# Kernel tuning notes

Measured on AMD Instinct MI355X. Metric: run time of the kernel, lower is better.

Reference implementation:

```python
import jax, jax.numpy as jnp
import numpy as np

B, S, E, H, MLP = 2, 2048, 1024, 16, 4096
VEC = 8          # args.vec_length: block-row height of vector-sparse mask
SPARSITY = 0.9   # fraction of attention entries dropped
D = E // H


def _make_mask():
    # static_random_mask_aligned: each block-row of VEC query rows keeps a
    # random ~(1-sparsity) subset of key columns. Diagonal kept so every
    # softmax row is non-empty.
    rng = np.random.default_rng(0)
    block = rng.random((S // VEC, S)) < (1.0 - SPARSITY)   # [m, n]
    mask = np.repeat(block, VEC, axis=0)                   # [S, S]
    mask |= np.eye(S, dtype=bool)
    return jnp.asarray(mask)


def setup_inputs() -> dict:
    key = jax.random.key(0)
    ks = jax.random.split(key, 8)
    w = lambda k, shp: (0.02 * jax.random.normal(k, shp, dtype=jnp.float32))
    return {
        "x": jax.random.normal(ks[0], (B, S, E), dtype=jnp.float32),
        "mask": _make_mask(),                       # [S,S] bool, static
        "w_qkv": w(ks[1], (3 * E, E)),             # in_proj_weight
        "b_qkv": jnp.zeros((3 * E,), jnp.float32),
        "w_out": w(ks[2], (E, E)),                 # out_proj
        "b_out": jnp.zeros((E,), jnp.float32),
        "g1": jnp.ones((E,), jnp.float32), "beta1": jnp.zeros((E,), jnp.float32),
        "g2": jnp.ones((E,), jnp.float32), "beta2": jnp.zeros((E,), jnp.float32),
        "w1": w(ks[3], (MLP, E)), "bias1": jnp.zeros((MLP,), jnp.float32),
        "w2": w(ks[4], (E, MLP)), "bias2": jnp.zeros((E,), jnp.float32),
    }


def _layer_norm(x, g, b, eps=1e-5):
    mu = jnp.mean(x, axis=-1, keepdims=True)
    var = jnp.mean(jnp.square(x - mu), axis=-1, keepdims=True)
    return (x - mu) * jax.lax.rsqrt(var + eps) * g + b


def _sparse_mha(h, mask, w_qkv, b_qkv, w_out, b_out):
    qkv = jnp.einsum("bse,fe->bsf", h, w_qkv) + b_qkv       # [B,S,3E]
    q, k, v = jnp.split(qkv, 3, axis=-1)
    q = q.reshape(B, S, H, D)
    k = k.reshape(B, S, H, D)
    v = v.reshape(B, S, H, D)
    scores = jnp.einsum("bqhd,bkhd->bhqk", q, k) / jnp.sqrt(jnp.float32(D))
    scores = jnp.where(mask[None, None], scores, jnp.float32(-1e9))
    p = jax.nn.softmax(scores, axis=-1)
    ctx = jnp.einsum("bhqk,bkhd->bqhd", p, v).reshape(B, S, E)
    return jnp.einsum("bse,fe->bsf", ctx, w_out) + b_out


def reference(x, mask, w_qkv, b_qkv, w_out, b_out, g1, beta1, g2, beta2,
              w1, bias1, w2, bias2):
    h = _layer_norm(x, g1, beta1)
    attn = _sparse_mha(h, mask, w_qkv, b_qkv, w_out, b_out)
    out = attn + x                      # residual 1
    out = _layer_norm(out, g2, beta2)
    out = jnp.einsum("bse,me->bsm", out, w1) + bias1   # linear1 (no activation, as in source)
    out = jnp.einsum("bsm,em->bse", out, w2) + bias2   # linear2
    return out + x                      # residual adds ORIGINAL x (as in source)
```

## Files before the change

### kernel.cpp

```cpp
#include <hip/hip_runtime.h>
#include <cstdint>
#include <cstddef>

typedef unsigned short u16;
typedef unsigned int u32;
typedef short s16x8 __attribute__((ext_vector_type(8)));
typedef float f32x4 __attribute__((ext_vector_type(4)));
typedef _Float16 f16x2 __attribute__((ext_vector_type(2)));

__device__ __forceinline__ float fdot2(f16x2 a, f16x2 b, float c) {
#if defined(__HIP_DEVICE_COMPILE__) && __has_builtin(__builtin_amdgcn_fdot2)
  return __builtin_amdgcn_fdot2(a, b, c, false);
#else
  return (float)a.x * (float)b.x + (float)a.y * (float)b.y + c;
#endif
}

__device__ __forceinline__ float red8(float x) {
#if defined(__HIP_DEVICE_COMPILE__)
  asm("v_add_f32_dpp %0, %0, %0 quad_perm:[1,0,3,2] row_mask:0xf bank_mask:0xf"
      : "+v"(x));
  asm("v_add_f32_dpp %0, %0, %0 quad_perm:[2,3,0,1] row_mask:0xf bank_mask:0xf"
      : "+v"(x));
  asm("v_add_f32_dpp %0, %0, %0 row_half_mirror row_mask:0xf bank_mask:0xf"
      : "+v"(x));
  return x;
#else
  x += __shfl_xor(x, 1); x += __shfl_xor(x, 2); x += __shfl_xor(x, 4);
  return x;
#endif
}

__device__ __forceinline__ void fmamix_lo(float& a, u32 hv, float p) {
#if defined(__HIP_DEVICE_COMPILE__)
  asm("v_fma_mix_f32 %0, %1, %2, %0 op_sel_hi:[1,0,0]"
      : "+v"(a) : "v"(hv), "v"(p));
#else
  union { u32 i; _Float16 h[2]; } c; c.i = hv; a += (float)c.h[0] * p;
#endif
}
__device__ __forceinline__ void fmamix_hi(float& a, u32 hv, float p) {
#if defined(__HIP_DEVICE_COMPILE__)
  asm("v_fma_mix_f32 %0, %1, %2, %0 op_sel:[1,0,0] op_sel_hi:[1,0,0]"
      : "+v"(a) : "v"(hv), "v"(p));
#else
  union { u32 i; _Float16 h[2]; } c; c.i = hv; a += (float)c.h[1] * p;
#endif
}

#define S_LEN 2048
#define EMB   1024
#define NHEAD 16
#define HD    64
#define E3    3072
#define MLPD  4096
#define NROWS 4096
#define LCAP  640

__device__ __forceinline__ float bf2f(u16 v) {
  union { u32 i; float f; } c; c.i = ((u32)v) << 16; return c.f;
}
__device__ __forceinline__ u16 f2bf(float f) {
  union { float f; u32 i; } c; c.f = f;
  u32 x = c.i;
  return (u16)((x + 0x7FFFu + ((x >> 16) & 1u)) >> 16);
}
__device__ __forceinline__ u16 f2h(float f) {
  _Float16 h = (_Float16)f;
  union { _Float16 h; u16 b; } c; c.h = h; return c.b;
}

__device__ __forceinline__ void gl2lds16(const void* g, void* l) {
  __builtin_amdgcn_global_load_lds(
      (__attribute__((address_space(1))) void*)(g),
      (__attribute__((address_space(3))) void*)(l), 16, 0, 0);
}

__global__ void detect_flags(const u32* __restrict__ w1s, int* __restrict__ dtflag,
                             const u32* __restrict__ mask, int* __restrict__ maskrep) {
  __shared__ int hits[256];
  __shared__ u32 red[256];
  int h = 0; u32 v = 0;
  for (int i = threadIdx.x; i < 4096; i += 256) {
    u32 w = w1s[i];
    if ((w & 0xFFFFu) && (((w >> 7) & 0xFFu) >= 0xC8u)) ++h;
    v |= mask[i];
  }
  hits[threadIdx.x] = h; red[threadIdx.x] = v;
  __syncthreads();
  if (threadIdx.x == 0) {
    int t = 0; u32 o = 0;
    for (int i = 0; i < 256; ++i) { t += hits[i]; o |= red[i]; }
    *dtflag = (t > 8) ? 1 : 0;
    int rep;
    if (o <= 1u) rep = 0;
    else if (o & 0x80u) rep = 1;
    else if (o & 0x00800000u) rep = 2;
    else rep = 3;
    *maskrep = rep;
  }
}

__device__ __forceinline__ bool maskbit(const void* m, int rep, size_t idx) {
  switch (rep) {
    case 0:  return ((const int*)m)[idx] != 0;
    case 1:  return ((const u16*)m)[idx] != 0;
    case 2:  return ((const u32*)m)[idx] != 0;
    default: return ((const unsigned char*)m)[idx] != 0;
  }
}

__global__ __launch_bounds__(256)
void cvt_kernel(const void* __restrict__ src, u16* __restrict__ dst,
                int n8, const int* __restrict__ dtflag) {
  const int i = blockIdx.x * blockDim.x + threadIdx.x;
  if (i >= n8) return;
  if (*dtflag) {
    const float4 a = ((const float4*)src)[i * 2];
    const float4 b = ((const float4*)src)[i * 2 + 1];
    u16 o[8] = {f2bf(a.x), f2bf(a.y), f2bf(a.z), f2bf(a.w),
                f2bf(b.x), f2bf(b.y), f2bf(b.z), f2bf(b.w)};
    *(uint4*)(dst + (size_t)i * 8) = *(const uint4*)o;
  } else {
    ((uint4*)dst)[i] = ((const uint4*)src)[i];
  }
}

__global__ void cvt_small(const void* s0, u16* d0, const void* s1, u16* d1,
                          const void* s2, u16* d2, const void* s3, u16* d3,
                          const void* s4, u16* d4, const void* s5, u16* d5,
                          const void* s6, u16* d6, const void* s7, u16* d7,
                          const int* __restrict__ dtflag) {
  const int f = *dtflag;
  const void* srcs[8] = {s0, s1, s2, s3, s4, s5, s6, s7};
  u16* dsts[8] = {d0, d1, d2, d3, d4, d5, d6, d7};
  const int ns[8] = {E3, EMB, EMB, EMB, EMB, EMB, MLPD, EMB};
#pragma unroll
  for (int k = 0; k < 8; ++k) {
    for (int idx = threadIdx.x; idx < ns[k]; idx += 256)
      dsts[k][idx] = f ? f2bf(((const float*)srcs[k])[idx])
                       : ((const u16*)srcs[k])[idx];
  }
}

__global__ void build_lists(const void* __restrict__ mask, const int* __restrict__ repf,
                            int* __restrict__ lists, int* __restrict__ cnt,
                            unsigned char* __restrict__ diagflag) {
  __shared__ int num;
  const int m = blockIdx.x;
  if (threadIdx.x == 0) num = 0;
  __syncthreads();
  const int rep = *repf;
  const int row0 = m * 8;
  for (int j = threadIdx.x; j < S_LEN; j += 256) {
    int srcrow = (j == row0) ? (row0 + 1) : row0;
    bool bit = maskbit(mask, rep, (size_t)srcrow * S_LEN + j);
    if (j >= row0 && j < row0 + 8) diagflag[j] = bit ? 0 : 1;
    if (bit) {
      int p = atomicAdd(&num, 1);
      if (p < LCAP) lists[m * LCAP + p] = j * 4096;
    }
  }
  __syncthreads();
  if (threadIdx.x == 0) cnt[m] = (num < LCAP) ? num : LCAP;
}

__global__ __launch_bounds__(256)
void ln_kernel(const void* __restrict__ Xv, const u16* __restrict__ g,
               const u16* __restrict__ be, u16* __restrict__ O,
               const int* __restrict__ inf32) {
  const int wv = threadIdx.x >> 6, ln = threadIdx.x & 63;
  const int row = blockIdx.x * 4 + wv;
  float v[16];
  if (inf32 && *inf32) {
    const float* xr = (const float*)Xv + (size_t)row * EMB;
    float4 a0 = *(const float4*)(xr + ln * 8);
    float4 a1 = *(const float4*)(xr + ln * 8 + 4);
    float4 b0 = *(const float4*)(xr + 512 + ln * 8);
    float4 b1 = *(const float4*)(xr + 512 + ln * 8 + 4);
    v[0]=a0.x; v[1]=a0.y; v[2]=a0.z; v[3]=a0.w; v[4]=a1.x; v[5]=a1.y; v[6]=a1.z; v[7]=a1.w;
    v[8]=b0.x; v[9]=b0.y; v[10]=b0.z; v[11]=b0.w; v[12]=b1.x; v[13]=b1.y; v[14]=b1.z; v[15]=b1.w;
  } else {
    const u16* xr = (const u16*)Xv + (size_t)row * EMB;
    union { uint4 u; u16 s[8]; } p0, p1;
    p0.u = *(const uint4*)(xr + ln * 8);
    p1.u = *(const uint4*)(xr + 512 + ln * 8);
#pragma unroll
    for (int t = 0; t < 8; ++t) { v[t] = bf2f(p0.s[t]); v[8 + t] = bf2f(p1.s[t]); }
  }
  float s = 0.f, sq = 0.f;
#pragma unroll
  for (int t = 0; t < 16; ++t) { s += v[t]; sq += v[t] * v[t]; }
#pragma unroll
  for (int off = 32; off; off >>= 1) { s += __shfl_xor(s, off); sq += __shfl_xor(sq, off); }
  const float mu = s * (1.0f / EMB);
  const float var = sq * (1.0f / EMB) - mu * mu;
  const float rsig = rsqrtf(var + 1e-5f);
  union { uint4 u; u16 s[8]; } g0, g1v, b0, b1v, o0, o1;
  g0.u = *(const uint4*)(g + ln * 8);   g1v.u = *(const uint4*)(g + 512 + ln * 8);
  b0.u = *(const uint4*)(be + ln * 8);  b1v.u = *(const uint4*)(be + 512 + ln * 8);
#pragma unroll
  for (int t = 0; t < 8; ++t) {
    o0.s[t] = f2bf((v[t]     - mu) * rsig * bf2f(g0.s[t])  + bf2f(b0.s[t]));
    o1.s[t] = f2bf((v[8 + t] - mu) * rsig * bf2f(g1v.s[t]) + bf2f(b1v.s[t]));
  }
  u16* orow = O + (size_t)row * EMB;
  *(uint4*)(orow + ln * 8) = o0.u;
  *(uint4*)(orow + 512 + ln * 8) = o1.u;
}

__global__ __launch_bounds__(256)
void gemm_bt(const u16* __restrict__ A, const u16* __restrict__ B,
             const u16* __restrict__ bias, u16* __restrict__ C,
             int M, int N, int K) {
  __shared__ u16 a_sh[128 * 64];
  __shared__ u16 b_sh[128 * 64];
  const int tid = threadIdx.x;
  const int wv = tid >> 6, ln = tid & 63;
  const int wm = wv & 1, wn = wv >> 1;
  const int tm = blockIdx.y, tn = blockIdx.x;
  const int srow = ln >> 3;
  const int scol = ((ln & 7) ^ srow) * 8;
  const int q = ln >> 4, rr = ln & 15;

  f32x4 acc[4][4] = {};
  const u16* Abase = A + (size_t)(tm * 128) * K;
  const u16* Bbase = B + (size_t)(tn * 128) * K;

  for (int k0 = 0; k0 < K; k0 += 64) {
    __syncthreads();
#pragma unroll
    for (int c = 0; c < 4; ++c) {
      const int chunk = wv * 4 + c;
      const int row = chunk * 8 + srow;
      gl2lds16(Abase + (size_t)row * K + k0 + scol, &a_sh[chunk * 512]);
      gl2lds16(Bbase + (size_t)row * K + k0 + scol, &b_sh[chunk * 512]);
    }
    __syncthreads();
#pragma unroll
    for (int kk = 0; kk < 2; ++kk) {
      const int slot = ((kk * 4 + q) ^ (rr & 7)) * 8;
      s16x8 af[4], bfr[4];
#pragma unroll
      for (int mi = 0; mi < 4; ++mi)
        af[mi] = *(const s16x8*)&a_sh[(wm * 64 + mi * 16 + rr) * 64 + slot];
#pragma unroll
      for (int ni = 0; ni < 4; ++ni)
        bfr[ni] = *(const s16x8*)&b_sh[(wn * 64 + ni * 16 + rr) * 64 + slot];
#pragma unroll
      for (int mi = 0; mi < 4; ++mi)
#pragma unroll
        for (int ni = 0; ni < 4; ++ni)
          acc[mi][ni] = __builtin_amdgcn_mfma_f32_16x16x32_bf16(af[mi], bfr[ni], acc[mi][ni], 0, 0, 0);
    }
  }
#pragma unroll
  for (int ni = 0; ni < 4; ++ni) {
    const int col = tn * 128 + wn * 64 + ni * 16 + rr;
    const float bv = bf2f(bias[col]);
#pragma unroll
    for (int mi = 0; mi < 4; ++mi)
#pragma unroll
      for (int r2 = 0; r2 < 4; ++r2) {
        const int row = tm * 128 + wm * 64 + mi * 16 + q * 4 + r2;
        C[(size_t)row * N + col] = f2bf(acc[mi][ni][r2] + bv);
      }
  }
}

__global__ __launch_bounds__(256)
void gemm_bt_sk(const u16* __restrict__ A, const u16* __restrict__ B,
                u16* __restrict__ P0, u16* __restrict__ P1,
                int M, int N, int K) {
  __shared__ u16 a_sh[128 * 64];
  __shared__ u16 b_sh[128 * 64];
  const int tid = threadIdx.x;
  const int wv = tid >> 6, ln = tid & 63;
  const int wm = wv & 1, wn = wv >> 1;
  const int tm = blockIdx.y, tn = blockIdx.x, kz = blockIdx.z;
  const int Kh = K >> 1;
  const int koff = kz * Kh;
  const int srow = ln >> 3;
  const int scol = ((ln & 7) ^ srow) * 8;
  const int q = ln >> 4, rr = ln & 15;

  f32x4 acc[4][4] = {};
  const u16* Abase = A + (size_t)(tm * 128) * K + koff;
  const u16* Bbase = B + (size_t)(tn * 128) * K + koff;

  for (int k0 = 0; k0 < Kh; k0 += 64) {
    __syncthreads();
#pragma unroll
    for (int c = 0; c < 4; ++c) {
      const int chunk = wv * 4 + c;
      const int row = chunk * 8 + srow;
      gl2lds16(Abase + (size_t)row * K + k0 + scol, &a_sh[chunk * 512]);
      gl2lds16(Bbase + (size_t)row * K + k0 + scol, &b_sh[chunk * 512]);
    }
    __syncthreads();
#pragma unroll
    for (int kk = 0; kk < 2; ++kk) {
      const int slot = ((kk * 4 + q) ^ (rr & 7)) * 8;
      s16x8 af[4], bfr[4];
#pragma unroll
      for (int mi = 0; mi < 4; ++mi)
        af[mi] = *(const s16x8*)&a_sh[(wm * 64 + mi * 16 + rr) * 64 + slot];
#pragma unroll
      for (int ni = 0; ni < 4; ++ni)
        bfr[ni] = *(const s16x8*)&b_sh[(wn * 64 + ni * 16 + rr) * 64 + slot];
#pragma unroll
      for (int mi = 0; mi < 4; ++mi)
#pragma unroll
        for (int ni = 0; ni < 4; ++ni)
          acc[mi][ni] = __builtin_amdgcn_mfma_f32_16x16x32_bf16(af[mi], bfr[ni], acc[mi][ni], 0, 0, 0);
    }
  }
  u16* P = kz ? P1 : P0;
#pragma unroll
  for (int ni = 0; ni < 4; ++ni) {
    const int col = tn * 128 + wn * 64 + ni * 16 + rr;
#pragma unroll
    for (int mi = 0; mi < 4; ++mi)
#pragma unroll
      for (int r2 = 0; r2 < 4; ++r2) {
        const int row = tm * 128 + wm * 64 + mi * 16 + q * 4 + r2;
        P[(size_t)row * N + col] = f2bf(acc[mi][ni][r2]);
      }
  }
}

__global__ __launch_bounds__(256)
void combine_kernel(const u16* __restrict__ P0, const u16* __restrict__ P1,
                    const u16* __restrict__ bias, const void* __restrict__ xr,
                    void* __restrict__ Ov, const int* __restrict__ f32io) {
  const int i = blockIdx.x * 256 + threadIdx.x;
  const int col8 = (i & 127) * 8;
  union { uint4 u; u16 s[8]; } a, b, bi;
  a.u = ((const uint4*)P0)[i];
  b.u = ((const uint4*)P1)[i];
  bi.u = *(const uint4*)(bias + col8);
  const int f = *f32io;
  float o[8];
#pragma unroll
  for (int t = 0; t < 8; ++t) o[t] = bf2f(a.s[t]) + bf2f(b.s[t]) + bf2f(bi.s[t]);
  if (f) {
    const float4 x0 = ((const float4*)xr)[i * 2];
    const float4 x1 = ((const float4*)xr)[i * 2 + 1];
    o[0]+=x0.x; o[1]+=x0.y; o[2]+=x0.z; o[3]+=x0.w;
    o[4]+=x1.x; o[5]+=x1.y; o[6]+=x1.z; o[7]+=x1.w;
    float4 r0 = {o[0],o[1],o[2],o[3]}, r1 = {o[4],o[5],o[6],o[7]};
    ((float4*)Ov)[i * 2] = r0;
    ((float4*)Ov)[i * 2 + 1] = r1;
  } else {
    union { uint4 u; u16 s[8]; } xv;
    xv.u = ((const uint4*)xr)[i];
    u16 r[8];
#pragma unroll
    for (int t = 0; t < 8; ++t) r[t] = f2bf(o[t] + bf2f(xv.s[t]));
    ((uint4*)Ov)[i] = *(const uint4*)r;
  }
}

__global__ __launch_bounds__(256)
void gemm_qkv(const u16* __restrict__ A, const u16* __restrict__ B,
              const u16* __restrict__ bias,
              u16* __restrict__ Qb, u16* __restrict__ KVp,
              int K) {
  __shared__ u16 a_sh[128 * 64];
  __shared__ u16 b_sh[128 * 64];
  const int tid = threadIdx.x;
  const int wv = tid >> 6, ln = tid & 63;
  const int wm = wv & 1, wn = wv >> 1;
  const int tm = blockIdx.y, tn = blockIdx.x;
  const int srow = ln >> 3;
  const int scol = ((ln & 7) ^ srow) * 8;
  const int q = ln >> 4, rr = ln & 15;

  f32x4 acc[4][4] = {};
  const u16* Abase = A + (size_t)(tm * 128) * K;
  const u16* Bbase = B + (size_t)(tn * 128) * K;

  for (int k0 = 0; k0 < K; k0 += 64) {
    __syncthreads();
#pragma unroll
    for (int c = 0; c < 4; ++c) {
      const int chunk = wv * 4 + c;
      const int row = chunk * 8 + srow;
      gl2lds16(Abase + (size_t)row * K + k0 + scol, &a_sh[chunk * 512]);
      gl2lds16(Bbase + (size_t)row * K + k0 + scol, &b_sh[chunk * 512]);
    }
    __syncthreads();
#pragma unroll
    for (int kk = 0; kk < 2; ++kk) {
      const int slot = ((kk * 4 + q) ^ (rr & 7)) * 8;
      s16x8 af[4], bfr[4];
#pragma unroll
      for (int mi = 0; mi < 4; ++mi)
        af[mi] = *(const s16x8*)&a_sh[(wm * 64 + mi * 16 + rr) * 64 + slot];
#pragma unroll
      for (int ni = 0; ni < 4; ++ni)
        bfr[ni] = *(const s16x8*)&b_sh[(wn * 64 + ni * 16 + rr) * 64 + slot];
#pragma unroll
      for (int mi = 0; mi < 4; ++mi)
#pragma unroll
        for (int ni = 0; ni < 4; ++ni)
          acc[mi][ni] = __builtin_amdgcn_mfma_f32_16x16x32_bf16(af[mi], bfr[ni], acc[mi][ni], 0, 0, 0);
    }
  }
  const int third = (tn * 128) >> 10;
#pragma unroll
  for (int ni = 0; ni < 4; ++ni) {
    const int col = tn * 128 + wn * 64 + ni * 16 + rr;
    const int w = col & 1023;
    const float bv = bf2f(bias[col]);
#pragma unroll
    for (int mi = 0; mi < 4; ++mi)
#pragma unroll
      for (int r2 = 0; r2 < 4; ++r2) {
        const int row = tm * 128 + wm * 64 + mi * 16 + q * 4 + r2;
        const float o = acc[mi][ni][r2] + bv;
        if (third == 0) {
          Qb[(size_t)row * 1024 + w] = f2bf(o);
        } else {
          const int hh = w >> 6, d = w & 63;
          KVp[(size_t)row * 2048 + hh * 128 + ((third == 1) ? 0 : 64) + d] = f2h(o);
        }
      }
  }
}

__global__ __launch_bounds__(256)
void gemm_bt_n64(const u16* __restrict__ A, const u16* __restrict__ B,
                 const u16* __restrict__ bias, const void* __restrict__ resid,
                 void* __restrict__ Cv, int M, int N, int K,
                 const int* __restrict__ residf32, const int* __restrict__ outf32) {
  __shared__ u16 a_sh[128 * 64];
  __shared__ u16 b_sh[64 * 64];
  const int tid = threadIdx.x;
  const int wv = tid >> 6, ln = tid & 63;
  const int wm = wv & 1, wn = wv >> 1;
  const int tm = blockIdx.y, tn = blockIdx.x;
  const int srow = ln >> 3;
  const int scol = ((ln & 7) ^ srow) * 8;
  const int q = ln >> 4, rr = ln & 15;

  f32x4 acc[4][2] = {};
  const u16* Abase = A + (size_t)(tm * 128) * K;
  const u16* Bbase = B + (size_t)(tn * 64) * K;

  for (int k0 = 0; k0 < K; k0 += 64) {
    __syncthreads();
#pragma unroll
    for (int c = 0; c < 4; ++c) {
      const int chunk = wv * 4 + c;
      const int row = chunk * 8 + srow;
      gl2lds16(Abase + (size_t)row * K + k0 + scol, &a_sh[chunk * 512]);
    }
#pragma unroll
    for (int c = 0; c < 2; ++c) {
      const int chunk = wv * 2 + c;
      const int row = chunk * 8 + srow;
      gl2lds16(Bbase + (size_t)row * K + k0 + scol, &b_sh[chunk * 512]);
    }
    __syncthreads();
#pragma unroll
    for (int kk = 0; kk < 2; ++kk) {
      const int slot = ((kk * 4 + q) ^ (rr & 7)) * 8;
      s16x8 af[4], bfr[2];
#pragma unroll
      for (int mi = 0; mi < 4; ++mi)
        af[mi] = *(const s16x8*)&a_sh[(wm * 64 + mi * 16 + rr) * 64 + slot];
#pragma unroll
      for (int ni = 0; ni < 2; ++ni)
        bfr[ni] = *(const s16x8*)&b_sh[(wn * 32 + ni * 16 + rr) * 64 + slot];
#pragma unroll
      for (int mi = 0; mi < 4; ++mi)
#pragma unroll
        for (int ni = 0; ni < 2; ++ni)
          acc[mi][ni] = __builtin_amdgcn_mfma_f32_16x16x32_bf16(af[mi], bfr[ni], acc[mi][ni], 0, 0, 0);
    }
  }
  const int rf32 = residf32 ? *residf32 : 0;
  const int f32o = outf32 ? *outf32 : 0;
#pragma unroll
  for (int ni = 0; ni < 2; ++ni) {
    const int col = tn * 64 + wn * 32 + ni * 16 + rr;
    const float bv = bf2f(bias[col]);
#pragma unroll
    for (int mi = 0; mi < 4; ++mi)
#pragma unroll
      for (int r2 = 0; r2 < 4; ++r2) {
        const int row = tm * 128 + wm * 64 + mi * 16 + q * 4 + r2;
        const size_t idx = (size_t)row * N + col;
        float o = acc[mi][ni][r2] + bv;
        if (resid)
          o += rf32 ? ((const float*)resid)[idx] : bf2f(((const u16*)resid)[idx]);
        if (f32o) ((float*)Cv)[idx] = o;
        else      ((u16*)Cv)[idx] = f2bf(o);
      }
  }
}

__global__ __launch_bounds__(128)
void attn_kernel(const u16* __restrict__ Qb, const u16* __restrict__ KVp,
                 const int* __restrict__ lists,
                 const int* __restrict__ cnt, const unsigned char* __restrict__ diagflag,
                 u16* __restrict__ ctx) {
  __shared__ int list_sh[LCAP];
  const int g = blockIdx.x;
  const int b = g >> 12;
  const int h = (g >> 8) & 15;
  const int m = g & 255;
  const int tid = threadIdx.x, wv = tid >> 6, ln = tid & 63;
  const int es = ln >> 3, dc = ln & 7;
  const int i0 = m * 8 + wv * 4;
  const int n = cnt[m];

  for (int e = tid; e < n; e += 128) list_sh[e] = lists[m * LCAP + e];
  __syncthreads();

  const float qs = 0.125f * 1.44269504f;
  f16x2 q[4][4];
#pragma unroll
  for (int r = 0; r < 4; ++r) {
    const u16* qrow = Qb + (size_t)(b * S_LEN + i0 + r) * EMB + h * 64 + dc * 8;
    union { uint4 u; u16 s[8]; } qi; qi.u = *(const uint4*)qrow;
#pragma unroll
    for (int t = 0; t < 4; ++t) {
      q[r][t].x = (_Float16)(bf2f(qi.s[2 * t])     * qs);
      q[r][t].y = (_Float16)(bf2f(qi.s[2 * t + 1]) * qs);
    }
  }

  const char* kvb = (const char*)KVp + (size_t)b * S_LEN * 4096;
  const u32 loff = (u32)(h * 256 + dc * 16);

  float sum[4] = {};
  float acc[4][8] = {};

  auto score1 = [&](const uint4& ku, int r) -> float {
    union { uint4 u; f16x2 kk[4]; } K; K.u = ku;
    float s = 0.f;
    if (r == 0) s = fdot2(K.kk[3], q[0][3], fdot2(K.kk[2], q[0][2],
                   fdot2(K.kk[1], q[0][1], fdot2(K.kk[0], q[0][0], 0.f))));
    else if (r == 1) s = fdot2(K.kk[3], q[1][3], fdot2(K.kk[2], q[1][2],
                   fdot2(K.kk[1], q[1][1], fdot2(K.kk[0], q[1][0], 0.f))));
    else if (r == 2) s = fdot2(K.kk[3], q[2][3], fdot2(K.kk[2], q[2][2],
                   fdot2(K.kk[1], q[2][1], fdot2(K.kk[0], q[2][0], 0.f))));
    else s = fdot2(K.kk[3], q[3][3], fdot2(K.kk[2], q[3][2],
                   fdot2(K.kk[1], q[3][1], fdot2(K.kk[0], q[3][0], 0.f))));
    s = red8(s);
    s = fminf(fmaxf(s, -126.f), 126.f);
    return exp2f(s);
  };

  auto PROC = [&](const uint4& ku, const uint4& vu) {
#pragma unroll
    for (int r = 0; r < 4; ++r) {
      const float p = score1(ku, r);
      sum[r] += p;
      fmamix_lo(acc[r][0], vu.x, p); fmamix_hi(acc[r][1], vu.x, p);
      fmamix_lo(acc[r][2], vu.y, p); fmamix_hi(acc[r][3], vu.y, p);
      fmamix_lo(acc[r][4], vu.z, p); fmamix_hi(acc[r][5], vu.z, p);
      fmamix_lo(acc[r][6], vu.w, p); fmamix_hi(acc[r][7], vu.w, p);
    }
  };

#pragma unroll
  for (int r = 0; r < 4; ++r) {
    if (diagflag[i0 + r]) {
      const u32 off = (u32)((i0 + r) * 4096) + loff;
      const uint4 ku = *(const uint4*)(kvb + off);
      const uint4 vu = *(const uint4*)(kvb + off + 128);
      float p = score1(ku, r);
      p = (es == 0) ? p : 0.f;
      sum[r] += p;
      fmamix_lo(acc[r][0], vu.x, p); fmamix_hi(acc[r][1], vu.x, p);
      fmamix_lo(acc[r][2], vu.y, p); fmamix_hi(acc[r][3], vu.y, p);
      fmamix_lo(acc[r][4], vu.z, p); fmamix_hi(acc[r][5], vu.z, p);
      fmamix_lo(acc[r][6], vu.w, p); fmamix_hi(acc[r][7], vu.w, p);
    }
  }

  int e0 = 0;
  if (n >= 16) {
    uint4 k0, v0, k1, v1;
    {
      const u32 o0 = (u32)list_sh[es] + loff;
      const u32 o1 = (u32)list_sh[8 + es] + loff;
      k0 = *(const uint4*)(kvb + o0); v0 = *(const uint4*)(kvb + o0 + 128);
      k1 = *(const uint4*)(kvb + o1); v1 = *(const uint4*)(kvb + o1 + 128);
    }
    for (; e0 + 32 <= n; e0 += 16) {
      const u32 o0 = (u32)list_sh[e0 + 16 + es] + loff;
      const u32 o1 = (u32)list_sh[e0 + 24 + es] + loff;
      const uint4 nk0 = *(const uint4*)(kvb + o0), nv0 = *(const uint4*)(kvb + o0 + 128);
      const uint4 nk1 = *(const uint4*)(kvb + o1), nv1 = *(const uint4*)(kvb + o1 + 128);
      PROC(k0, v0);
      PROC(k1, v1);
      k0 = nk0; v0 = nv0; k1 = nk1; v1 = nv1;
    }
    PROC(k0, v0);
    PROC(k1, v1);
    e0 += 16;
  }
  for (; e0 + 8 <= n; e0 += 8) {
    const u32 o = (u32)list_sh[e0 + es] + loff;
    const uint4 ku = *(const uint4*)(kvb + o);
    const uint4 vu = *(const uint4*)(kvb + o + 128);
    PROC(ku, vu);
  }
  if (e0 < n) {
    const int e = e0 + es;
    const bool valid = (e < n);
    const u32 o = (u32)(valid ? list_sh[e] : list_sh[0]) + loff;
    const uint4 ku = *(const uint4*)(kvb + o);
    const uint4 vu = *(const uint4*)(kvb + o + 128);
#pragma unroll
    for (int r = 0; r < 4; ++r) {
      float p = score1(ku, r);
      p = valid ? p : 0.f;
      sum[r] += p;
      fmamix_lo(acc[r][0], vu.x, p); fmamix_hi(acc[r][1], vu.x, p);
      fmamix_lo(acc[r][2], vu.y, p); fmamix_hi(acc[r][3], vu.y, p);
      fmamix_lo(acc[r][4], vu.z, p); fmamix_hi(acc[r][5], vu.z, p);
      fmamix_lo(acc[r][6], vu.w, p); fmamix_hi(acc[r][7], vu.w, p);
    }
  }

#pragma unroll
  for (int off = 8; off < 64; off <<= 1) {
#pragma unroll
    for (int r = 0; r < 4; ++r) {
      sum[r] += __shfl_xor(sum[r], off);
#pragma unroll
      for (int t = 0; t < 8; ++t) acc[r][t] += __shfl_xor(acc[r][t], off);
    }
  }

  if (es == 0) {
#pragma unroll
    for (int r = 0; r < 4; ++r) {
      const float inv = 1.0f / sum[r];
      u16 o[8];
#pragma unroll
      for (int t = 0; t < 8; ++t) o[t] = f2bf(acc[r][t] * inv);
      *(uint4*)(ctx + (size_t)(b * S_LEN + i0 + r) * EMB + h * 64 + dc * 8) = *(const uint4*)o;
    }
  }
}

extern "C" void kernel_launch(void* const* d_in, const int* in_sizes, int n_in,
                              void* d_out, int out_size, void* d_ws, size_t ws_size,
                              hipStream_t stream) {
  const void* x_raw    = d_in[0];
  const void* mask     = d_in[1];
  const void* wqkv_raw = d_in[2];
  const void* bqkv_raw = d_in[3];
  const void* wout_raw = d_in[4];
  const void* bout_raw = d_in[5];
  const void* g1_raw   = d_in[6];
  const void* be1_raw  = d_in[7];
  const void* g2_raw   = d_in[8];
  const void* be2_raw  = d_in[9];
  const void* w1_raw   = d_in[10];
  const void* b1_raw   = d_in[11];
  const void* w2_raw   = d_in[12];
  const void* b2_raw   = d_in[13];

  char* ws = (char*)d_ws;
  const size_t MB = 1u << 20;
  int* dtflag         = (int*)ws;
  int* maskrep        = (int*)(ws + 64);
  int* cnt            = (int*)(ws + 1024);
  unsigned char* dfl  = (unsigned char*)(ws + 4096);
  int* lists          = (int*)(ws + 8192);
  u16* R1  = (u16*)(ws + 1 * MB);
  u16* Qb  = (u16*)(ws + 9 * MB);
  u16* KVp = (u16*)(ws + 17 * MB);
  u16* M1  = (u16*)(ws + 17 * MB);
  u16* W   = (u16*)(ws + 49 * MB);
  char* sm = ws + 57 * MB;
  u16* bq  = (u16*)(sm);
  u16* bo  = (u16*)(sm + 8192);
  u16* g1b = (u16*)(sm + 16384);
  u16* be1b= (u16*)(sm + 24576);
  u16* g2b = (u16*)(sm + 32768);
  u16* be2b= (u16*)(sm + 40960);
  u16* b1b = (u16*)(sm + 49152);
  u16* b2b = (u16*)(sm + 65536);

  detect_flags<<<dim3(1), dim3(256), 0, stream>>>((const u32*)w1_raw, dtflag,
                                                  (const u32*)mask, maskrep);
  build_lists<<<dim3(256), dim3(256), 0, stream>>>(mask, maskrep, lists, cnt, dfl);
  cvt_small<<<dim3(1), dim3(256), 0, stream>>>(
      bqkv_raw, bq, bout_raw, bo, g1_raw, g1b, be1_raw, be1b,
      g2_raw, g2b, be2_raw, be2b, b1_raw, b1b, b2_raw, b2b, dtflag);

  auto cvt = [&](const void* src, u16* dst, int n) {
    const int n8 = n / 8;
    cvt_kernel<<<dim3((n8 + 255) / 256), dim3(256), 0, stream>>>(src, dst, n8, dtflag);
  };

  ln_kernel<<<dim3(NROWS / 4), dim3(256), 0, stream>>>(x_raw, g1b, be1b, R1, dtflag);
  cvt(wqkv_raw, W, E3 * EMB);
  gemm_qkv<<<dim3(E3 / 128, NROWS / 128), dim3(256), 0, stream>>>(
      R1, W, bq, Qb, KVp, EMB);
  attn_kernel<<<dim3(2 * NHEAD * 256), dim3(128), 0, stream>>>(
      Qb, KVp, lists, cnt, dfl, R1);
  cvt(wout_raw, W, EMB * EMB);
  gemm_bt_n64<<<dim3(EMB / 64, NROWS / 128), dim3(256), 0, stream>>>(
      R1, W, bo, x_raw, Qb, NROWS, EMB, EMB, dtflag, nullptr);
  ln_kernel<<<dim3(NROWS / 4), dim3(256), 0, stream>>>(Qb, g2b, be2b, R1, nullptr);
  cvt(w1_raw, W, MLPD * EMB);
  gemm_bt<<<dim3(MLPD / 128, NROWS / 128), dim3(256), 0, stream>>>(
      R1, W, b1b, M1, NROWS, MLPD, EMB);
  cvt(w2_raw, W, EMB * MLPD);
  gemm_bt_sk<<<dim3(EMB / 128, NROWS / 128, 2), dim3(256), 0, stream>>>(
      M1, W, R1, Qb, NROWS, EMB, MLPD);
  combine_kernel<<<dim3(NROWS * EMB / 8 / 256), dim3(256), 0, stream>>>(
      R1, Qb, b2b, x_raw, d_out, dtflag);
}
```

Measured before the change: 430.1 us.

## Give each attention wave a full 8-row block-row and pack four block-rows per workgroup

Previously two waves split one 8-row block-row, so each gathered the same K/V columns for four query rows. Now each wave handles all eight rows of its block-row, so every gathered K/V vector is reused across eight queries. This halves K/V gather traffic, and a 256-thread workgroup holds four block-rows with separate shared lists. The cost is double the register use for accumulators (8x8 acc plus 8x4 q), which may lower occupancy or spill, and waves within a workgroup may be imbalanced because list lengths differ per block-row.

```diff
diff --git a/kernel.cpp b/kernel.cpp
--- a/kernel.cpp
+++ b/kernel.cpp
@@ -501,28 +501,34 @@
   }
 }
 
-__global__ __launch_bounds__(128)
+__global__ __launch_bounds__(256)
 void attn_kernel(const u16* __restrict__ Qb, const u16* __restrict__ KVp,
                  const int* __restrict__ lists,
                  const int* __restrict__ cnt, const unsigned char* __restrict__ diagflag,
                  u16* __restrict__ ctx) {
-  __shared__ int list_sh[LCAP];
+  __shared__ int list_sh[4][LCAP];
   const int g = blockIdx.x;
-  const int b = g >> 12;
-  const int h = (g >> 8) & 15;
-  const int m = g & 255;
+  const int b = g >> 10;
+  const int h = (g >> 6) & 15;
+  const int mq = g & 63;
   const int tid = threadIdx.x, wv = tid >> 6, ln = tid & 63;
   const int es = ln >> 3, dc = ln & 7;
-  const int i0 = m * 8 + wv * 4;
+  const int m = mq * 4 + wv;
+  const int i0 = m * 8;
+
+#pragma unroll
+  for (int w = 0; w < 4; ++w) {
+    const int nw = cnt[mq * 4 + w];
+    for (int e = tid; e < nw; e += 256) list_sh[w][e] = lists[(mq * 4 + w) * LCAP + e];
+  }
+  __syncthreads();
+
   const int n = cnt[m];
 
-  for (int e = tid; e < n; e += 128) list_sh[e] = lists[m * LCAP + e];
-  __syncthreads();
-
   const float qs = 0.125f * 1.44269504f;
-  f16x2 q[4][4];
-#pragma unroll
-  for (int r = 0; r < 4; ++r) {
+  f16x2 q[8][4];
+#pragma unroll
+  for (int r = 0; r < 8; ++r) {
     const u16* qrow = Qb + (size_t)(b * S_LEN + i0 + r) * EMB + h * 64 + dc * 8;
     union { uint4 u; u16 s[8]; } qi; qi.u = *(const uint4*)qrow;
 #pragma unroll
@@ -535,20 +541,13 @@
   const char* kvb = (const char*)KVp + (size_t)b * S_LEN * 4096;
   const u32 loff = (u32)(h * 256 + dc * 16);
 
-  float sum[4] = {};
-  float acc[4][8] = {};
-
-  auto score1 = [&](const uint4& ku, int r) -> float {
+  float sum[8] = {};
+  float acc[8][8] = {};
+
+  auto scoreq = [&](const uint4& ku, const f16x2 (&qq)[4]) -> float {
     union { uint4 u; f16x2 kk[4]; } K; K.u = ku;
-    float s = 0.f;
-    if (r == 0) s = fdot2(K.kk[3], q[0][3], fdot2(K.kk[2], q[0][2],
-                   fdot2(K.kk[1], q[0][1], fdot2(K.kk[0], q[0][0], 0.f))));
-    else if (r == 1) s = fdot2(K.kk[3], q[1][3], fdot2(K.kk[2], q[1][2],
-                   fdot2(K.kk[1], q[1][1], fdot2(K.kk[0], q[1][0], 0.f))));
-    else if (r == 2) s = fdot2(K.kk[3], q[2][3], fdot2(K.kk[2], q[2][2],
-                   fdot2(K.kk[1], q[2][1], fdot2(K.kk[0], q[2][0], 0.f))));
-    else s = fdot2(K.kk[3], q[3][3], fdot2(K.kk[2], q[3][2],
-                   fdot2(K.kk[1], q[3][1], fdot2(K.kk[0], q[3][0], 0.f))));
+    float s = fdot2(K.kk[3], qq[3], fdot2(K.kk[2], qq[2],
+              fdot2(K.kk[1], qq[1], fdot2(K.kk[0], qq[0], 0.f))));
     s = red8(s);
     s = fminf(fmaxf(s, -126.f), 126.f);
     return exp2f(s);
@@ -556,8 +555,8 @@
 
   auto PROC = [&](const uint4& ku, const uint4& vu) {
 #pragma unroll
-    for (int r = 0; r < 4; ++r) {
-      const float p = score1(ku, r);
+    for (int r = 0; r < 8; ++r) {
+      const float p = scoreq(ku, q[r]);
       sum[r] += p;
       fmamix_lo(acc[r][0], vu.x, p); fmamix_hi(acc[r][1], vu.x, p);
       fmamix_lo(acc[r][2], vu.y, p); fmamix_hi(acc[r][3], vu.y, p);
@@ -567,12 +566,12 @@
   };
 
 #pragma unroll
-  for (int r = 0; r < 4; ++r) {
+  for (int r = 0; r < 8; ++r) {
     if (diagflag[i0 + r]) {
       const u32 off = (u32)((i0 + r) * 4096) + loff;
       const uint4 ku = *(const uint4*)(kvb + off);
       const uint4 vu = *(const uint4*)(kvb + off + 128);
-      float p = score1(ku, r);
+      float p = scoreq(ku, q[r]);
       p = (es == 0) ? p : 0.f;
       sum[r] += p;
       fmamix_lo(acc[r][0], vu.x, p); fmamix_hi(acc[r][1], vu.x, p);
@@ -586,14 +585,14 @@
   if (n >= 16) {
     uint4 k0, v0, k1, v1;
     {
-      const u32 o0 = (u32)list_sh[es] + loff;
-      const u32 o1 = (u32)list_sh[8 + es] + loff;
+      const u32 o0 = (u32)list_sh[wv][es] + loff;
+      const u32 o1 = (u32)list_sh[wv][8 + es] + loff;
       k0 = *(const uint4*)(kvb + o0); v0 = *(const uint4*)(kvb + o0 + 128);
       k1 = *(const uint4*)(kvb + o1); v1 = *(const uint4*)(kvb + o1 + 128);
     }
     for (; e0 + 32 <= n; e0 += 16) {
-      const u32 o0 = (u32)list_sh[e0 + 16 + es] + loff;
-      const u32 o1 = (u32)list_sh[e0 + 24 + es] + loff;
+      const u32 o0 = (u32)list_sh[wv][e0 + 16 + es] + loff;
+      const u32 o1 = (u32)list_sh[wv][e0 + 24 + es] + loff;
       const uint4 nk0 = *(const uint4*)(kvb + o0), nv0 = *(const uint4*)(kvb + o0 + 128);
       const uint4 nk1 = *(const uint4*)(kvb + o1), nv1 = *(const uint4*)(kvb + o1 + 128);
       PROC(k0, v0);
@@ -605,7 +604,7 @@
     e0 += 16;
   }
   for (; e0 + 8 <= n; e0 += 8) {
-    const u32 o = (u32)list_sh[e0 + es] + loff;
+    const u32 o = (u32)list_sh[wv][e0 + es] + loff;
     const uint4 ku = *(const uint4*)(kvb + o);
     const uint4 vu = *(const uint4*)(kvb + o + 128);
     PROC(ku, vu);
@@ -613,12 +612,12 @@
   if (e0 < n) {
     const int e = e0 + es;
     const bool valid = (e < n);
-    const u32 o = (u32)(valid ? list_sh[e] : list_sh[0]) + loff;
+    const u32 o = (u32)(valid ? list_sh[wv][e] : list_sh[wv][0]) + loff;
     const uint4 ku = *(const uint4*)(kvb + o);
     const uint4 vu = *(const uint4*)(kvb + o + 128);
 #pragma unroll
-    for (int r = 0; r < 4; ++r) {
-      float p = score1(ku, r);
+    for (int r = 0; r < 8; ++r) {
+      float p = scoreq(ku, q[r]);
       p = valid ? p : 0.f;
       sum[r] += p;
       fmamix_lo(acc[r][0], vu.x, p); fmamix_hi(acc[r][1], vu.x, p);
@@ -631,7 +630,7 @@
 #pragma unroll
   for (int off = 8; off < 64; off <<= 1) {
 #pragma unroll
-    for (int r = 0; r < 4; ++r) {
+    for (int r = 0; r < 8; ++r) {
       sum[r] += __shfl_xor(sum[r], off);
 #pragma unroll
       for (int t = 0; t < 8; ++t) acc[r][t] += __shfl_xor(acc[r][t], off);
@@ -640,7 +639,7 @@
 
   if (es == 0) {
 #pragma unroll
-    for (int r = 0; r < 4; ++r) {
+    for (int r = 0; r < 8; ++r) {
       const float inv = 1.0f / sum[r];
       u16 o[8];
 #pragma unroll
@@ -706,7 +705,7 @@
   cvt(wqkv_raw, W, E3 * EMB);
   gemm_qkv<<<dim3(E3 / 128, NROWS / 128), dim3(256), 0, stream>>>(
       R1, W, bq, Qb, KVp, EMB);
-  attn_kernel<<<dim3(2 * NHEAD * 256), dim3(128), 0, stream>>>(
+  attn_kernel<<<dim3(2 * NHEAD * 64), dim3(256), 0, stream>>>(
       Qb, KVp, lists, cnt, dfl, R1);
   cvt(wout_raw, W, EMB * EMB);
   gemm_bt_n64<<<dim3(EMB / 64, NROWS / 128), dim3(256), 0, stream>>>(
```

New measurement: 445.2 us. 3.5% more time.
